# Kernel tuning notes

Hardware: AMD Instinct MI355X
Metric: run time of the kernel (lower is better)

Reference implementation:

```python
import jax, jax.numpy as jnp
import numpy as np

B, K, M, L = 16, 256, 16, 64
DET_C, HID, H, DEPTH = 1152, 128, 4, 2
DK = HID // H
SCALE = np.float32(1.0 / np.sqrt(DK))


def _ln(x, g, b):
    mu = jnp.mean(x, -1, keepdims=True)
    v = jnp.mean((x - mu) ** 2, -1, keepdims=True)
    return (x - mu) * jax.lax.rsqrt(v + 1e-5) * g + b


def _bn(x, g, b, m, v):  # eval-mode BatchNorm1d, channel-last
    return (x - m) * (g * jax.lax.rsqrt(v + 1e-5)) + b


def _prelu(x, a):
    return jnp.where(x >= 0, x, a * x)


def _mha(q_in, k_in, v_in, Wq, bq, Wk, bk, Wv, bv, Wo, bo, lg, lb, bias=None, mask=None):
    # MultiHeadAttention: scaled dot-product + residual + LayerNorm (eval, no dropout)
    Bb, Nq, _ = q_in.shape
    Nk = k_in.shape[1]
    q = (q_in @ Wq.T + bq).reshape(Bb, Nq, H, DK).transpose(0, 2, 1, 3)
    k = (k_in @ Wk.T + bk).reshape(Bb, Nk, H, DK).transpose(0, 2, 1, 3)
    v = (v_in @ Wv.T + bv).reshape(Bb, Nk, H, DK).transpose(0, 2, 1, 3)
    att = jnp.einsum('bhqd,bhkd->bhqk', q, k) * SCALE
    if bias is not None:
        att = att + bias  # way='add': per-head distance bias
    if mask is not None:
        att = jnp.where(mask, jnp.float32(-1e9), att)
    att = jax.nn.softmax(att, axis=-1)
    out = jnp.einsum('bhqk,bhkd->bhqd', att, v).transpose(0, 2, 1, 3).reshape(Bb, Nq, HID)
    out = out @ Wo.T + bo
    return _ln(q_in + out, lg, lb)


def setup_inputs() -> dict:
    key = jax.random.key(0)
    ks = iter(jax.random.split(key, 64))
    def nrm(shape, s=0.05):
        return jax.random.normal(next(ks), shape, jnp.float32) * s
    d = {}
    d['center'] = jax.random.normal(next(ks), (B, K, 3), jnp.float32)
    d['detr_features'] = nrm((B, K, DET_C), 1.0)
    d['lang_fea'] = nrm((B * M, L, HID), 1.0)
    d['fc_W1'] = nrm((HID, DET_C)); d['fc_b1'] = jnp.zeros((HID,), jnp.float32)
    for pre in ['bn1', 'mbn1', 'mbn2']:
        d[pre + '_g'] = jnp.ones((HID,), jnp.float32)
        d[pre + '_b'] = jnp.zeros((HID,), jnp.float32)
        d[pre + '_m'] = jnp.zeros((HID,), jnp.float32)
        d[pre + '_v'] = jnp.ones((HID,), jnp.float32)
    d['pr1_a'] = 0.25 * jnp.ones((HID,), jnp.float32)
    d['fc_W2'] = nrm((HID, HID)); d['fc_b2'] = jnp.zeros((HID,), jnp.float32)
    for pre in ['sa', 'ca']:
        for nm in ['Wq', 'Wk', 'Wv', 'Wo']:
            d[f'{pre}_{nm}'] = nrm((DEPTH, HID, HID))
        for nm in ['bq', 'bk', 'bv', 'bo', 'lb']:
            d[f'{pre}_{nm}'] = jnp.zeros((DEPTH, HID), jnp.float32)
        d[f'{pre}_lg'] = jnp.ones((DEPTH, HID), jnp.float32)
    d['m_W1'] = nrm((HID, HID)); d['m_b1'] = jnp.zeros((HID,), jnp.float32)
    d['mp1_a'] = 0.25 * jnp.ones((1,), jnp.float32)
    d['m_W2'] = nrm((HID, HID)); d['m_b2'] = jnp.zeros((HID,), jnp.float32)
    d['mp2_a'] = 0.25 * jnp.ones((1,), jnp.float32)
    d['m_W3'] = nrm((1, HID)); d['m_b3'] = jnp.zeros((1,), jnp.float32)
    d['attention_mask'] = jax.random.bernoulli(next(ks), 0.2, (B * M, 1, 1, L))
    d['len_nun_max'] = M
    return d


def reference(center, detr_features, lang_fea,
              fc_W1, fc_b1, bn1_g, bn1_b, bn1_m, bn1_v, pr1_a, fc_W2, fc_b2,
              sa_Wq, sa_bq, sa_Wk, sa_bk, sa_Wv, sa_bv, sa_Wo, sa_bo, sa_lg, sa_lb,
              ca_Wq, ca_bq, ca_Wk, ca_bk, ca_Wv, ca_bv, ca_Wo, ca_bo, ca_lg, ca_lb,
              m_W1, m_b1, mbn1_g, mbn1_b, mbn1_m, mbn1_v, mp1_a,
              m_W2, m_b2, mbn2_g, mbn2_b, mbn2_m, mbn2_v, mp2_a,
              m_W3, m_b3, attention_mask, len_nun_max):
    # distance-based attention bias (detached in the original)
    c = jax.lax.stop_gradient(center)
    dist = jnp.sqrt(jnp.sum((c[:, None, :, :] - c[:, :, None, :]) ** 2, -1))[:, None]  # (B,1,K,K)
    dw = 1.0 / (dist + 0.01)
    dw = dw / jnp.sum(dw, axis=2, keepdims=True)
    zeros = jnp.zeros_like(dw)
    dist_weights = jnp.concatenate([dw, -dist, zeros, zeros], axis=1)  # (B,H,K,K), one bias per head

    # features_concat: Conv1d(1x1) + BN + PReLU + Conv1d(1x1), channel-last
    x = detr_features @ fc_W1.T + fc_b1
    x = _prelu(_bn(x, bn1_g, bn1_b, bn1_m, bn1_v), pr1_a)
    x = x @ fc_W2.T + fc_b2  # (B,K,HID)

    feats = _mha(x, x, x, sa_Wq[0], sa_bq[0], sa_Wk[0], sa_bk[0], sa_Wv[0], sa_bv[0],
                 sa_Wo[0], sa_bo[0], sa_lg[0], sa_lb[0], bias=dist_weights)

    m = int(len_nun_max)
    feats = jnp.broadcast_to(feats[:, None], (B, m, K, HID)).reshape(B * m, K, HID)
    dwb = jnp.broadcast_to(dist_weights[:, None], (B, m, H, K, K)).reshape(B * m, H, K, K)

    f1 = _mha(feats, lang_fea, lang_fea, ca_Wq[0], ca_bq[0], ca_Wk[0], ca_bk[0], ca_Wv[0],
              ca_bv[0], ca_Wo[0], ca_bo[0], ca_lg[0], ca_lb[0], mask=attention_mask)
    for i in range(1, DEPTH):
        f1 = _mha(f1, f1, f1, sa_Wq[i], sa_bq[i], sa_Wk[i], sa_bk[i], sa_Wv[i], sa_bv[i],
                  sa_Wo[i], sa_bo[i], sa_lg[i], sa_lb[i], bias=dwb)
        f1 = _mha(f1, lang_fea, lang_fea, ca_Wq[i], ca_bq[i], ca_Wk[i], ca_bk[i], ca_Wv[i],
                  ca_bv[i], ca_Wo[i], ca_bo[i], ca_lg[i], ca_lb[i], mask=attention_mask)

    # match head: conv1x1+BN+PReLU x2 + conv1x1 -> 1
    y = f1 @ m_W1.T + m_b1
    y = _prelu(_bn(y, mbn1_g, mbn1_b, mbn1_m, mbn1_v), mp1_a)
    y = y @ m_W2.T + m_b2
    y = _prelu(_bn(y, mbn2_g, mbn2_b, mbn2_m, mbn2_v), mp2_a)
    conf = (y @ m_W3.T + m_b3)[..., 0]  # (B*M, K) cluster_ref
    return conf
```

## Files before the change

kernel.cpp:

```cpp
#include <hip/hip_runtime.h>
#include <hip/hip_bf16.h>
#include <cstdio>

#define KQ   256
#define HID  128
typedef unsigned short u16;
#define SCALE_F 0.1767766952966369f

typedef __bf16 bf16x8 __attribute__((ext_vector_type(8)));
typedef short  s16x8  __attribute__((ext_vector_type(8)));
typedef float  f32x4  __attribute__((ext_vector_type(4)));

static __device__ __forceinline__ float bfu(u16 u) {
    return __uint_as_float(((unsigned)u) << 16);
}
static __device__ __forceinline__ u16 f2b(float f) {
    unsigned u = __float_as_uint(f);
    return (u16)((u + 0x7FFFu + ((u >> 16) & 1u)) >> 16);
}
static __device__ __forceinline__ float ldf(const void* p, int i, int f) {
    return f ? ((const float*)p)[i] : bfu(((const u16*)p)[i]);
}
static __device__ __forceinline__ f32x4 mfma16(s16x8 a, s16x8 b, f32x4 c) {
    return __builtin_amdgcn_mfma_f32_16x16x32_bf16(
        __builtin_bit_cast(bf16x8, a), __builtin_bit_cast(bf16x8, b), c, 0, 0, 0);
}

#define OFF_WB     8256
#define OFF_LANGB  237632
#define OFF_DWB    1286208
#define OFF_DIST   2334784
#define OFF_ROWS   3383360
#define OFF_FEATSB 3387456
#define OFF_FAB    3649600
#define OFF_QB     7843904
#define OFF_KB     12038208
#define OFF_VB     16232512
#define OFF_MASK   20426816
#define NEEDF      20430912

#define WB_FCW1 0
#define WB_FCW2 147456
#define WB_SAWQ 163840
#define WB_SAWK 196608
#define WB_SAWV 229376
#define WB_SAWO 262144
#define WB_CAWQ 294912
#define WB_CAWK 327680
#define WB_CAWV 360448
#define WB_CAWO 393216
#define WB_MW1  425984
#define WB_MW2  442368

__global__ __launch_bounds__(256) void k_detect(
    const unsigned* __restrict__ onesw, const unsigned* __restrict__ maskw,
    int* __restrict__ flags)
{
    __shared__ int fb;
    if (threadIdx.x == 0) fb = 0;
    __syncthreads();
    int any = 0;
    for (int i = threadIdx.x; i < 4096; i += 256) any |= (maskw[i] > 1u) ? 1 : 0;
    if (any) atomicOr(&fb, 1);
    __syncthreads();
    if (threadIdx.x == 0) {
        flags[0] = (onesw[0] == 0x3F800000u) ? 1 : 0;
        flags[1] = fb;
    }
}

__global__ __launch_bounds__(256) void k_mask_canon(
    const unsigned char* __restrict__ raw, const int* __restrict__ flags,
    unsigned char* __restrict__ mask8)
{
    int i = blockIdx.x*256 + threadIdx.x;
    if (flags[1]) mask8[i] = raw[i] ? 1 : 0;
    else          mask8[i] = (((const unsigned int*)raw)[i] != 0u) ? 1 : 0;
}

__global__ __launch_bounds__(256) void k_cv16(
    const void* __restrict__ src, u16* __restrict__ dst, int n,
    const int* __restrict__ flags)
{
    int i = (blockIdx.x*256 + threadIdx.x)*4;
    if (i >= n) return;
    if (flags[0]) {
        float4 v = *(const float4*)((const float*)src + i);
        ushort4 o; o.x = f2b(v.x); o.y = f2b(v.y); o.z = f2b(v.z); o.w = f2b(v.w);
        *(ushort4*)(dst + i) = o;
    } else {
        *(ushort4*)(dst + i) = *(const ushort4*)((const u16*)src + i);
    }
}

__global__ __launch_bounds__(256) void k_rowsum(
    const void* __restrict__ center, float* __restrict__ rowsum,
    const int* __restrict__ flags)
{
    int f  = flags[0];
    int bi = blockIdx.x, b = bi >> 8, j = threadIdx.x;
    float cx = ldf(center, bi*3+0, f), cy = ldf(center, bi*3+1, f), cz = ldf(center, bi*3+2, f);
    int pj = (b << 8) + j;
    float px = ldf(center, pj*3+0, f), py = ldf(center, pj*3+1, f), pz = ldf(center, pj*3+2, f);
    float dx = px-cx, dy = py-cy, dz = pz-cz;
    float d  = sqrtf(dx*dx + dy*dy + dz*dz);
    float w  = 1.f/(d + 0.01f);
    float sw = w;
    #pragma unroll
    for (int m = 32; m >= 1; m >>= 1) sw += __shfl_xor(sw, m);
    __shared__ float red[4];
    if ((j & 63) == 0) red[j >> 6] = sw;
    __syncthreads();
    if (j == 0) rowsum[bi] = red[0] + red[1] + red[2] + red[3];
}

template<int EPI, bool ABCAST, bool RBCAST>
__global__ __launch_bounds__(256) void k_gemm(
    const u16* __restrict__ A, const u16* __restrict__ W, u16* __restrict__ C,
    int Kd, const void* __restrict__ bias,
    const void* __restrict__ bng, const void* __restrict__ bnb,
    const void* __restrict__ bnm, const void* __restrict__ bnv,
    const void* __restrict__ pa,
    const void* __restrict__ lg, const void* __restrict__ lb,
    const u16* __restrict__ resid, const int* __restrict__ flags, int voff)
{
    __shared__ __align__(16) u16 Wl[128*136];
    int f = flags[0];
    int t = threadIdx.x, w = t>>6, lane = t&63, lm = lane&15, q4 = lane>>4;
    int m0 = blockIdx.x*64;
    int arow = m0 + w*16 + lm;
    int grow = ABCAST ? (((arow>>12)<<8)|(arow&255)) : arow;
    const u16* Abase = A + (size_t)grow*Kd;
    f32x4 acc[8];
    #pragma unroll
    for (int nt = 0; nt < 8; ++nt) acc[nt] = f32x4{0.f,0.f,0.f,0.f};
    int sr = t>>1, ss = (t&1)*64;
    for (int k0 = 0; k0 < Kd; k0 += 128) {
        const u16* src = W + (size_t)sr*Kd + k0 + ss;
        u16* dst = Wl + sr*136 + ss;
        #pragma unroll
        for (int i = 0; i < 8; ++i) *(s16x8*)(dst + i*8) = *(const s16x8*)(src + i*8);
        __syncthreads();
        s16x8 aF[4];
        #pragma unroll
        for (int ks = 0; ks < 4; ++ks) aF[ks] = *(const s16x8*)(Abase + k0 + ks*32 + q4*8);
        #pragma unroll
        for (int nt = 0; nt < 8; ++nt)
            #pragma unroll
            for (int ks = 0; ks < 4; ++ks) {
                s16x8 bF = *(const s16x8*)(Wl + (nt*16+lm)*136 + ks*32 + q4*8);
                acc[nt] = mfma16(aF[ks], bF, acc[nt]);
            }
        __syncthreads();
    }
    int row = m0 + w*16 + q4*4;
    if (EPI == 3) {
        float xs[8][4];
        #pragma unroll
        for (int nt = 0; nt < 8; ++nt) {
            int ch = nt*16 + lm;
            float bs = ldf(bias, voff + ch, f);
            #pragma unroll
            for (int r = 0; r < 4; ++r) {
                int rr = row + r;
                int rrow = RBCAST ? (((rr>>12)<<8)|(rr&255)) : rr;
                xs[nt][r] = acc[nt][r] + bs + bfu(resid[(size_t)rrow*HID + ch]);
            }
        }
        #pragma unroll
        for (int r = 0; r < 4; ++r) {
            float sm = 0.f, sq = 0.f;
            #pragma unroll
            for (int nt = 0; nt < 8; ++nt) { sm += xs[nt][r]; sq += xs[nt][r]*xs[nt][r]; }
            #pragma unroll
            for (int d = 1; d <= 8; d <<= 1) { sm += __shfl_xor(sm, d); sq += __shfl_xor(sq, d); }
            float mean = sm * (1.f/128.f);
            float var  = sq * (1.f/128.f) - mean*mean;
            float rs   = rsqrtf(var + 1e-5f);
            #pragma unroll
            for (int nt = 0; nt < 8; ++nt) {
                int ch = nt*16 + lm;
                float g = ldf(lg, voff + ch, f), bb = ldf(lb, voff + ch, f);
                C[(size_t)(row+r)*HID + ch] = f2b((xs[nt][r]-mean)*rs*g + bb);
            }
        }
    } else {
        #pragma unroll
        for (int nt = 0; nt < 8; ++nt) {
            int ch = nt*16 + lm;
            float bs = ldf(bias, voff + ch, f);
            float scl = 1.f, sh = 0.f, al = 0.f;
            if (EPI >= 1) {
                float g  = ldf(bng, ch, f), bb = ldf(bnb, ch, f);
                float mn = ldf(bnm, ch, f), vv = ldf(bnv, ch, f);
                scl = g * rsqrtf(vv + 1e-5f);
                sh  = bb - mn*scl;
                al  = (EPI == 2) ? ldf(pa, 0, f) : ldf(pa, ch, f);
            }
            #pragma unroll
            for (int r = 0; r < 4; ++r) {
                float x = acc[nt][r] + bs;
                if (EPI >= 1) { x = x*scl + sh; x = (x >= 0.f) ? x : al*x; }
                C[(size_t)(row+r)*HID + ch] = f2b(x);
            }
        }
    }
}

__global__ __launch_bounds__(256) void k_sattn(
    const u16* __restrict__ Q, const u16* __restrict__ K, const u16* __restrict__ V,
    u16* __restrict__ O, const void* __restrict__ center,
    const float* __restrict__ rowsum, const int* __restrict__ flags, int bdiv)
{
    __shared__ __align__(16) u16 Kl[256*40];
    __shared__ __align__(16) u16 Vt[32*264];
    __shared__ __align__(16) u16 P[4][16*264];
    __shared__ float cxl[256], cyl[256], czl[256], rsl[256];
    int s = blockIdx.x, h = blockIdx.y;
    int t = threadIdx.x, w = t>>6, lane = t&63, lm = lane&15, q4 = lane>>4;
    int f = flags[0];
    int b = s / bdiv;
    {
        const u16* src = K + ((size_t)s*KQ + t)*HID + h*32;
        u16* dst = Kl + t*40;
        #pragma unroll
        for (int i = 0; i < 4; ++i) *(s16x8*)(dst + i*8) = *(const s16x8*)(src + i*8);
    }
    for (int idx = t; idx < 256*8; idx += 256) {
        int k = idx >> 3, d4 = idx & 7;
        ushort4 u = *(const ushort4*)(V + ((size_t)s*KQ + k)*HID + h*32 + d4*4);
        Vt[(d4*4+0)*264 + k] = u.x;
        Vt[(d4*4+1)*264 + k] = u.y;
        Vt[(d4*4+2)*264 + k] = u.z;
        Vt[(d4*4+3)*264 + k] = u.w;
    }
    {
        int j = (b << 8) + t;
        cxl[t] = ldf(center, j*3+0, f);
        cyl[t] = ldf(center, j*3+1, f);
        czl[t] = ldf(center, j*3+2, f);
        rsl[t] = rowsum[j];
    }
    __syncthreads();
    u16* Pw = P[w];
    for (int qt = 0; qt < 4; ++qt) {
        int qrow0 = qt*64 + w*16;
        s16x8 aq = *(const s16x8*)(Q + ((size_t)s*KQ + qrow0 + lm)*HID + h*32 + q4*8);
        float qx[4], qy[4], qz[4];
        if (h < 2) {
            #pragma unroll
            for (int r = 0; r < 4; ++r) {
                int q = qrow0 + q4*4 + r;
                qx[r] = cxl[q]; qy[r] = cyl[q]; qz[r] = czl[q];
            }
        }
        float S[16][4];
        #pragma unroll
        for (int kt = 0; kt < 16; ++kt) {
            s16x8 bF = *(const s16x8*)(Kl + (kt*16+lm)*40 + q4*8);
            f32x4 acc = f32x4{0.f,0.f,0.f,0.f};
            acc = mfma16(aq, bF, acc);
            int key = kt*16 + lm;
            float kx = 0.f, ky = 0.f, kz = 0.f, rs_ = 1.f;
            if (h < 2) { kx = cxl[key]; ky = cyl[key]; kz = czl[key]; rs_ = rsl[key]; }
            #pragma unroll
            for (int r = 0; r < 4; ++r) {
                float sc = acc[r]*SCALE_F;
                if (h < 2) {
                    float dx = qx[r]-kx, dy = qy[r]-ky, dz = qz[r]-kz;
                    float d  = sqrtf(dx*dx + dy*dy + dz*dz);
                    if (h == 0) sc += (1.f/(d + 0.01f)) / rs_;
                    else        sc -= d;
                }
                S[kt][r] = sc;
            }
        }
        float l[4];
        #pragma unroll
        for (int r = 0; r < 4; ++r) {
            float m = -3.0e38f;
            #pragma unroll
            for (int kt = 0; kt < 16; ++kt) m = fmaxf(m, S[kt][r]);
            #pragma unroll
            for (int d = 1; d <= 8; d <<= 1) m = fmaxf(m, __shfl_xor(m, d));
            float sum = 0.f;
            #pragma unroll
            for (int kt = 0; kt < 16; ++kt) { float p = __expf(S[kt][r]-m); S[kt][r] = p; sum += p; }
            #pragma unroll
            for (int d = 1; d <= 8; d <<= 1) sum += __shfl_xor(sum, d);
            l[r] = sum;
        }
        #pragma unroll
        for (int kt = 0; kt < 16; ++kt)
            #pragma unroll
            for (int r = 0; r < 4; ++r)
                Pw[(q4*4+r)*264 + kt*16 + lm] = f2b(S[kt][r]);
        #pragma unroll
        for (int nt = 0; nt < 2; ++nt) {
            f32x4 acc = f32x4{0.f,0.f,0.f,0.f};
            #pragma unroll
            for (int ks = 0; ks < 8; ++ks) {
                s16x8 ap = *(const s16x8*)(Pw + lm*264 + ks*32 + q4*8);
                s16x8 bv = *(const s16x8*)(Vt + (nt*16+lm)*264 + ks*32 + q4*8);
                acc = mfma16(ap, bv, acc);
            }
            #pragma unroll
            for (int r = 0; r < 4; ++r)
                O[((size_t)s*KQ + qrow0 + q4*4 + r)*HID + h*32 + nt*16 + lm] = f2b(acc[r] / l[r]);
        }
    }
}

__global__ __launch_bounds__(256) void k_xattn(
    const u16* __restrict__ Q, const u16* __restrict__ K, const u16* __restrict__ V,
    u16* __restrict__ O, const unsigned char* __restrict__ mask)
{
    __shared__ __align__(16) u16 Kl[64*40];
    __shared__ __align__(16) u16 Vt[32*72];
    __shared__ __align__(16) u16 P[4][16*72];
    __shared__ float madd[64];
    int s = blockIdx.x, h = blockIdx.y;
    int t = threadIdx.x, w = t>>6, lane = t&63, lm = lane&15, q4 = lane>>4;
    if (t < 64) {
        const u16* src = K + ((size_t)s*64 + t)*HID + h*32;
        u16* dst = Kl + t*40;
        #pragma unroll
        for (int i = 0; i < 4; ++i) *(s16x8*)(dst + i*8) = *(const s16x8*)(src + i*8);
        madd[t] = mask[s*64 + t] ? -1.0e9f : 0.f;
    }
    for (int idx = t; idx < 64*8; idx += 256) {
        int k = idx >> 3, d4 = idx & 7;
        ushort4 u = *(const ushort4*)(V + ((size_t)s*64 + k)*HID + h*32 + d4*4);
        Vt[(d4*4+0)*72 + k] = u.x;
        Vt[(d4*4+1)*72 + k] = u.y;
        Vt[(d4*4+2)*72 + k] = u.z;
        Vt[(d4*4+3)*72 + k] = u.w;
    }
    __syncthreads();
    u16* Pw = P[w];
    for (int qt = 0; qt < 4; ++qt) {
        int qrow0 = qt*64 + w*16;
        s16x8 aq = *(const s16x8*)(Q + ((size_t)s*KQ + qrow0 + lm)*HID + h*32 + q4*8);
        float S[4][4];
        #pragma unroll
        for (int kt = 0; kt < 4; ++kt) {
            s16x8 bF = *(const s16x8*)(Kl + (kt*16+lm)*40 + q4*8);
            f32x4 acc = f32x4{0.f,0.f,0.f,0.f};
            acc = mfma16(aq, bF, acc);
            float ma = madd[kt*16 + lm];
            #pragma unroll
            for (int r = 0; r < 4; ++r) S[kt][r] = acc[r]*SCALE_F + ma;
        }
        float l[4];
        #pragma unroll
        for (int r = 0; r < 4; ++r) {
            float m = -3.0e38f;
            #pragma unroll
            for (int kt = 0; kt < 4; ++kt) m = fmaxf(m, S[kt][r]);
            #pragma unroll
            for (int d = 1; d <= 8; d <<= 1) m = fmaxf(m, __shfl_xor(m, d));
            float sum = 0.f;
            #pragma unroll
            for (int kt = 0; kt < 4; ++kt) { float p = __expf(S[kt][r]-m); S[kt][r] = p; sum += p; }
            #pragma unroll
            for (int d = 1; d <= 8; d <<= 1) sum += __shfl_xor(sum, d);
            l[r] = sum;
        }
        #pragma unroll
        for (int kt = 0; kt < 4; ++kt)
            #pragma unroll
            for (int r = 0; r < 4; ++r)
                Pw[(q4*4+r)*72 + kt*16 + lm] = f2b(S[kt][r]);
        #pragma unroll
        for (int nt = 0; nt < 2; ++nt) {
            f32x4 acc = f32x4{0.f,0.f,0.f,0.f};
            #pragma unroll
            for (int ks = 0; ks < 2; ++ks) {
                s16x8 ap = *(const s16x8*)(Pw + lm*72 + ks*32 + q4*8);
                s16x8 bv = *(const s16x8*)(Vt + (nt*16+lm)*72 + ks*32 + q4*8);
                acc = mfma16(ap, bv, acc);
            }
            #pragma unroll
            for (int r = 0; r < 4; ++r)
                O[((size_t)s*KQ + qrow0 + q4*4 + r)*HID + h*32 + nt*16 + lm] = f2b(acc[r] / l[r]);
        }
    }
}

__global__ __launch_bounds__(256) void k_final(
    const u16* __restrict__ Y, const void* __restrict__ w3,
    const void* __restrict__ b3, void* __restrict__ outp,
    const int* __restrict__ flags)
{
    int f = flags[0];
    int w = threadIdx.x >> 6, lane = threadIdx.x & 63;
    int row = blockIdx.x*4 + w;
    float p = bfu(Y[(size_t)row*HID + lane])*ldf(w3, lane, f)
            + bfu(Y[(size_t)row*HID + 64 + lane])*ldf(w3, 64+lane, f);
    #pragma unroll
    for (int m = 32; m >= 1; m >>= 1) p += __shfl_xor(p, m);
    if (lane == 0) {
        float r = p + ldf(b3, 0, f);
        if (f) ((float*)outp)[row] = r;
        else   ((u16*)outp)[row]   = f2b(r);
    }
}

extern "C" void kernel_launch(void* const* d_in, const int* in_sizes, int n_in,
                              void* d_out, int out_size, void* d_ws, size_t ws_size,
                              hipStream_t stream)
{
    (void)n_in;
    if (ws_size < (size_t)NEEDF * 4) {
        fprintf(stderr, "kernel_launch: ws too small: have %zu need %zu\n",
                ws_size, (size_t)NEEDF * 4);
        hipMemsetAsync(d_out, 0, (size_t)out_size * 2, stream);
        return;
    }
    float* F = (float*)d_ws;
    u16*   U = (u16*)d_ws;
    int* flags = (int*)d_ws;
    u16* WB     = U + (size_t)OFF_WB*2;
    u16* langb  = U + (size_t)OFF_LANGB*2;
    u16* detrb  = U + (size_t)OFF_KB*2;
    u16* featsb = U + (size_t)OFF_FEATSB*2;
    u16* x2b    = U + (size_t)OFF_FAB*2;
    u16* fAb    = U + (size_t)OFF_FAB*2;
    u16* x1b    = U + (size_t)OFF_VB*2;
    u16* Qb     = U + (size_t)OFF_QB*2;
    u16* Kb     = U + (size_t)OFF_KB*2;
    u16* Vb     = U + (size_t)OFF_VB*2;
    float* rowsum = F + OFF_ROWS;
    unsigned char* mask8 = (unsigned char*)(F + OFF_MASK);

    k_detect<<<1, 256, 0, stream>>>((const unsigned*)d_in[8],
                                    (const unsigned*)d_in[48], flags);
    k_mask_canon<<<64, 256, 0, stream>>>((const unsigned char*)d_in[48], flags, mask8);

    struct { int idx; u16* dst; int n; } cv[14] = {
        {3,  WB+WB_FCW1, 147456}, {18, WB+WB_FCW2, 16384},
        {20, WB+WB_SAWQ, 32768}, {21, WB+WB_SAWK, 32768},
        {22, WB+WB_SAWV, 32768}, {23, WB+WB_SAWO, 32768},
        {30, WB+WB_CAWQ, 32768}, {31, WB+WB_CAWK, 32768},
        {32, WB+WB_CAWV, 32768}, {33, WB+WB_CAWO, 32768},
        {40, WB+WB_MW1, 16384},  {43, WB+WB_MW2, 16384},
        {1,  detrb, 4718592},    {2,  langb, 2097152},
    };
    for (int e = 0; e < 14; ++e)
        k_cv16<<<(cv[e].n + 1023)/1024, 256, 0, stream>>>(
            d_in[cv[e].idx], cv[e].dst, cv[e].n, flags);

    k_rowsum<<<4096, 256, 0, stream>>>(d_in[0], rowsum, flags);

    const void* N0 = nullptr;

    k_gemm<1,false,false><<<64, 256, 0, stream>>>(detrb, WB+WB_FCW1, x1b, 1152,
        d_in[4], d_in[5], d_in[6], d_in[7], d_in[8], d_in[17], N0, N0, nullptr, flags, 0);
    k_gemm<0,false,false><<<64, 256, 0, stream>>>(x1b, WB+WB_FCW2, x2b, 128,
        d_in[19], N0,N0,N0,N0,N0, N0, N0, nullptr, flags, 0);

    k_gemm<0,false,false><<<64, 256, 0, stream>>>(x2b, WB+WB_SAWQ, Qb, 128,
        d_in[24], N0,N0,N0,N0,N0, N0, N0, nullptr, flags, 0);
    k_gemm<0,false,false><<<64, 256, 0, stream>>>(x2b, WB+WB_SAWK, Kb, 128,
        d_in[25], N0,N0,N0,N0,N0, N0, N0, nullptr, flags, 0);
    k_gemm<0,false,false><<<64, 256, 0, stream>>>(x2b, WB+WB_SAWV, Vb, 128,
        d_in[26], N0,N0,N0,N0,N0, N0, N0, nullptr, flags, 0);
    k_sattn<<<dim3(16,4), 256, 0, stream>>>(Qb, Kb, Vb, Qb, d_in[0], rowsum, flags, 1);
    k_gemm<3,false,false><<<64, 256, 0, stream>>>(Qb, WB+WB_SAWO, featsb, 128,
        d_in[27], N0,N0,N0,N0,N0, d_in[29], d_in[28], x2b, flags, 0);

    k_gemm<0,true, false><<<1024, 256, 0, stream>>>(featsb, WB+WB_CAWQ, Qb, 128,
        d_in[34], N0,N0,N0,N0,N0, N0, N0, nullptr, flags, 0);
    k_gemm<0,false,false><<<256,  256, 0, stream>>>(langb, WB+WB_CAWK, Kb, 128,
        d_in[35], N0,N0,N0,N0,N0, N0, N0, nullptr, flags, 0);
    k_gemm<0,false,false><<<256,  256, 0, stream>>>(langb, WB+WB_CAWV, Vb, 128,
        d_in[36], N0,N0,N0,N0,N0, N0, N0, nullptr, flags, 0);
    k_xattn<<<dim3(256,4), 256, 0, stream>>>(Qb, Kb, Vb, Qb, mask8);
    k_gemm<3,false,true><<<1024, 256, 0, stream>>>(Qb, WB+WB_CAWO, fAb, 128,
        d_in[37], N0,N0,N0,N0,N0, d_in[39], d_in[38], featsb, flags, 0);

    k_gemm<0,false,false><<<1024, 256, 0, stream>>>(fAb, WB+WB_SAWQ+16384, Qb, 128,
        d_in[24], N0,N0,N0,N0,N0, N0, N0, nullptr, flags, 128);
    k_gemm<0,false,false><<<1024, 256, 0, stream>>>(fAb, WB+WB_SAWK+16384, Kb, 128,
        d_in[25], N0,N0,N0,N0,N0, N0, N0, nullptr, flags, 128);
    k_gemm<0,false,false><<<1024, 256, 0, stream>>>(fAb, WB+WB_SAWV+16384, Vb, 128,
        d_in[26], N0,N0,N0,N0,N0, N0, N0, nullptr, flags, 128);
    k_sattn<<<dim3(256,4), 256, 0, stream>>>(Qb, Kb, Vb, Qb, d_in[0], rowsum, flags, 16);
    k_gemm<3,false,false><<<1024, 256, 0, stream>>>(Qb, WB+WB_SAWO+16384, fAb, 128,
        d_in[27], N0,N0,N0,N0,N0, d_in[29], d_in[28], fAb, flags, 128);

    k_gemm<0,false,false><<<1024, 256, 0, stream>>>(fAb, WB+WB_CAWQ+16384, Qb, 128,
        d_in[34], N0,N0,N0,N0,N0, N0, N0, nullptr, flags, 128);
    k_gemm<0,false,false><<<256,  256, 0, stream>>>(langb, WB+WB_CAWK+16384, Kb, 128,
        d_in[35], N0,N0,N0,N0,N0, N0, N0, nullptr, flags, 128);
    k_gemm<0,false,false><<<256,  256, 0, stream>>>(langb, WB+WB_CAWV+16384, Vb, 128,
        d_in[36], N0,N0,N0,N0,N0, N0, N0, nullptr, flags, 128);
    k_xattn<<<dim3(256,4), 256, 0, stream>>>(Qb, Kb, Vb, Qb, mask8);
    k_gemm<3,false,false><<<1024, 256, 0, stream>>>(Qb, WB+WB_CAWO+16384, fAb, 128,
        d_in[37], N0,N0,N0,N0,N0, d_in[39], d_in[38], fAb, flags, 128);

    k_gemm<2,false,false><<<1024, 256, 0, stream>>>(fAb, WB+WB_MW1, Qb, 128,
        d_in[41], d_in[9], d_in[10], d_in[11], d_in[12], d_in[42], N0, N0, nullptr, flags, 0);
    k_gemm<2,false,false><<<1024, 256, 0, stream>>>(Qb, WB+WB_MW2, Kb, 128,
        d_in[44], d_in[13], d_in[14], d_in[15], d_in[16], d_in[45], N0, N0, nullptr, flags, 0);
    k_final<<<16384, 256, 0, stream>>>(Kb, d_in[46], d_in[47], d_out, flags);
}
```

Before: 614.7 us.

## Batch conversions, fuse QKV GEMMs, fold final projection into match GEMM

Replaces 14 separate conversion launches with one table-driven kernel, merges the Q/K/V (and cross-attention K/V) projection GEMMs into multi-output launches via a grid y-dimension, and fuses the final 128->1 projection into the second match-head GEMM epilogue, removing k_final. It also precomputes reciprocal row sums and swaps divisions for rcp multiplies in the attention kernels. The aim is to cut launch overhead and one full intermediate write/read, at the cost of fast-reciprocal precision and a branchy element lookup in the conversion kernel.

```diff
diff --git a/kernel.cpp b/kernel.cpp
--- a/kernel.cpp
+++ b/kernel.cpp
@@ -28,8 +28,6 @@
 
 #define OFF_WB     8256
 #define OFF_LANGB  237632
-#define OFF_DWB    1286208
-#define OFF_DIST   2334784
 #define OFF_ROWS   3383360
 #define OFF_FEATSB 3387456
 #define OFF_FAB    3649600
@@ -78,23 +76,30 @@
     else          mask8[i] = (((const unsigned int*)raw)[i] != 0u) ? 1 : 0;
 }
 
-__global__ __launch_bounds__(256) void k_cv16(
-    const void* __restrict__ src, u16* __restrict__ dst, int n,
-    const int* __restrict__ flags)
-{
-    int i = (blockIdx.x*256 + threadIdx.x)*4;
-    if (i >= n) return;
+struct CvTab {
+    const void* src[14];
+    unsigned long long dst[14];
+    int bstart[15];
+};
+__global__ __launch_bounds__(256) void k_convAll(
+    CvTab t, u16* __restrict__ U, const int* __restrict__ flags)
+{
+    int b = blockIdx.x;
+    int e = 0;
+    while (e < 13 && b >= t.bstart[e+1]) ++e;
+    long long local = (long long)(b - t.bstart[e])*1024 + threadIdx.x*4;
+    u16* dst = U + t.dst[e] + local;
     if (flags[0]) {
-        float4 v = *(const float4*)((const float*)src + i);
+        float4 v = *((const float4*)t.src[e] + (local >> 2));
         ushort4 o; o.x = f2b(v.x); o.y = f2b(v.y); o.z = f2b(v.z); o.w = f2b(v.w);
-        *(ushort4*)(dst + i) = o;
+        *(ushort4*)dst = o;
     } else {
-        *(ushort4*)(dst + i) = *(const ushort4*)((const u16*)src + i);
+        *(ushort4*)dst = *((const ushort4*)t.src[e] + (local >> 2));
     }
 }
 
 __global__ __launch_bounds__(256) void k_rowsum(
-    const void* __restrict__ center, float* __restrict__ rowsum,
+    const void* __restrict__ center, float* __restrict__ rsinv,
     const int* __restrict__ flags)
 {
     int f  = flags[0];
@@ -111,7 +116,7 @@
     __shared__ float red[4];
     if ((j & 63) == 0) red[j >> 6] = sw;
     __syncthreads();
-    if (j == 0) rowsum[bi] = red[0] + red[1] + red[2] + red[3];
+    if (j == 0) rsinv[bi] = 1.f / (red[0] + red[1] + red[2] + red[3]);
 }
 
 template<int EPI, bool ABCAST, bool RBCAST>
@@ -184,6 +189,39 @@
                 C[(size_t)(row+r)*HID + ch] = f2b((xs[nt][r]-mean)*rs*g + bb);
             }
         }
+    } else if (EPI == 4) {
+        float sum[4] = {0.f, 0.f, 0.f, 0.f};
+        float al = ldf(pa, 0, f);
+        #pragma unroll
+        for (int nt = 0; nt < 8; ++nt) {
+            int ch = nt*16 + lm;
+            float bs = ldf(bias, ch, f);
+            float g  = ldf(bng, ch, f), bb = ldf(bnb, ch, f);
+            float mn = ldf(bnm, ch, f), vv = ldf(bnv, ch, f);
+            float scl = g * rsqrtf(vv + 1e-5f);
+            float sh  = bb - mn*scl;
+            float w3v = ldf(lg, ch, f);
+            #pragma unroll
+            for (int r = 0; r < 4; ++r) {
+                float x = acc[nt][r] + bs;
+                x = x*scl + sh;
+                x = (x >= 0.f) ? x : al*x;
+                sum[r] += x * w3v;
+            }
+        }
+        #pragma unroll
+        for (int r = 0; r < 4; ++r)
+            #pragma unroll
+            for (int d = 1; d <= 8; d <<= 1) sum[r] += __shfl_xor(sum[r], d);
+        if (lm == 0) {
+            float b3v = ldf(lb, 0, f);
+            #pragma unroll
+            for (int r = 0; r < 4; ++r) {
+                float rr = sum[r] + b3v;
+                if (f) ((float*)C)[row + r] = rr;
+                else   C[row + r] = f2b(rr);
+            }
+        }
     } else {
         #pragma unroll
         for (int nt = 0; nt < 8; ++nt) {
@@ -207,10 +245,61 @@
     }
 }
 
+template<bool ABCAST>
+__global__ __launch_bounds__(256) void k_gemmN(
+    const u16* __restrict__ A,
+    const u16* __restrict__ W0, const u16* __restrict__ W1, const u16* __restrict__ W2,
+    u16* __restrict__ C0, u16* __restrict__ C1, u16* __restrict__ C2,
+    const void* __restrict__ b0, const void* __restrict__ b1, const void* __restrict__ b2,
+    const int* __restrict__ flags, int voff)
+{
+    __shared__ __align__(16) u16 Wl[128*136];
+    int y = blockIdx.y;
+    const u16* W = (y == 0) ? W0 : (y == 1) ? W1 : W2;
+    u16* C = (y == 0) ? C0 : (y == 1) ? C1 : C2;
+    const void* bias = (y == 0) ? b0 : (y == 1) ? b1 : b2;
+    int f = flags[0];
+    int t = threadIdx.x, w = t>>6, lane = t&63, lm = lane&15, q4 = lane>>4;
+    int m0 = blockIdx.x*64;
+    int arow = m0 + w*16 + lm;
+    int grow = ABCAST ? (((arow>>12)<<8)|(arow&255)) : arow;
+    const u16* Abase = A + (size_t)grow*128;
+    f32x4 acc[8];
+    #pragma unroll
+    for (int nt = 0; nt < 8; ++nt) acc[nt] = f32x4{0.f,0.f,0.f,0.f};
+    int sr = t>>1, ss = (t&1)*64;
+    {
+        const u16* src = W + (size_t)sr*128 + ss;
+        u16* dst = Wl + sr*136 + ss;
+        #pragma unroll
+        for (int i = 0; i < 8; ++i) *(s16x8*)(dst + i*8) = *(const s16x8*)(src + i*8);
+    }
+    __syncthreads();
+    s16x8 aF[4];
+    #pragma unroll
+    for (int ks = 0; ks < 4; ++ks) aF[ks] = *(const s16x8*)(Abase + ks*32 + q4*8);
+    #pragma unroll
+    for (int nt = 0; nt < 8; ++nt)
+        #pragma unroll
+        for (int ks = 0; ks < 4; ++ks) {
+            s16x8 bF = *(const s16x8*)(Wl + (nt*16+lm)*136 + ks*32 + q4*8);
+            acc[nt] = mfma16(aF[ks], bF, acc[nt]);
+        }
+    int row = m0 + w*16 + q4*4;
+    #pragma unroll
+    for (int nt = 0; nt < 8; ++nt) {
+        int ch = nt*16 + lm;
+        float bs = ldf(bias, voff + ch, f);
+        #pragma unroll
+        for (int r = 0; r < 4; ++r)
+            C[(size_t)(row+r)*HID + ch] = f2b(acc[nt][r] + bs);
+    }
+}
+
 __global__ __launch_bounds__(256) void k_sattn(
     const u16* __restrict__ Q, const u16* __restrict__ K, const u16* __restrict__ V,
     u16* __restrict__ O, const void* __restrict__ center,
-    const float* __restrict__ rowsum, const int* __restrict__ flags, int bdiv)
+    const float* __restrict__ rsinv, const int* __restrict__ flags, int bdiv)
 {
     __shared__ __align__(16) u16 Kl[256*40];
     __shared__ __align__(16) u16 Vt[32*264];
@@ -239,7 +328,7 @@
         cxl[t] = ldf(center, j*3+0, f);
         cyl[t] = ldf(center, j*3+1, f);
         czl[t] = ldf(center, j*3+2, f);
-        rsl[t] = rowsum[j];
+        rsl[t] = rsinv[j];
     }
     __syncthreads();
     u16* Pw = P[w];
@@ -269,13 +358,13 @@
                 if (h < 2) {
                     float dx = qx[r]-kx, dy = qy[r]-ky, dz = qz[r]-kz;
                     float d  = sqrtf(dx*dx + dy*dy + dz*dz);
-                    if (h == 0) sc += (1.f/(d + 0.01f)) / rs_;
+                    if (h == 0) sc += __builtin_amdgcn_rcpf(d + 0.01f) * rs_;
                     else        sc -= d;
                 }
                 S[kt][r] = sc;
             }
         }
-        float l[4];
+        float linv[4];
         #pragma unroll
         for (int r = 0; r < 4; ++r) {
             float m = -3.0e38f;
@@ -288,7 +377,7 @@
             for (int kt = 0; kt < 16; ++kt) { float p = __expf(S[kt][r]-m); S[kt][r] = p; sum += p; }
             #pragma unroll
             for (int d = 1; d <= 8; d <<= 1) sum += __shfl_xor(sum, d);
-            l[r] = sum;
+            linv[r] = __builtin_amdgcn_rcpf(sum);
         }
         #pragma unroll
         for (int kt = 0; kt < 16; ++kt)
@@ -306,7 +395,7 @@
             }
             #pragma unroll
             for (int r = 0; r < 4; ++r)
-                O[((size_t)s*KQ + qrow0 + q4*4 + r)*HID + h*32 + nt*16 + lm] = f2b(acc[r] / l[r]);
+                O[((size_t)s*KQ + qrow0 + q4*4 + r)*HID + h*32 + nt*16 + lm] = f2b(acc[r] * linv[r]);
         }
     }
 }
@@ -351,7 +440,7 @@
             #pragma unroll
             for (int r = 0; r < 4; ++r) S[kt][r] = acc[r]*SCALE_F + ma;
         }
-        float l[4];
+        float linv[4];
         #pragma unroll
         for (int r = 0; r < 4; ++r) {
             float m = -3.0e38f;
@@ -364,7 +453,7 @@
             for (int kt = 0; kt < 4; ++kt) { float p = __expf(S[kt][r]-m); S[kt][r] = p; sum += p; }
             #pragma unroll
             for (int d = 1; d <= 8; d <<= 1) sum += __shfl_xor(sum, d);
-            l[r] = sum;
+            linv[r] = __builtin_amdgcn_rcpf(sum);
         }
         #pragma unroll
         for (int kt = 0; kt < 4; ++kt)
@@ -382,27 +471,8 @@
             }
             #pragma unroll
             for (int r = 0; r < 4; ++r)
-                O[((size_t)s*KQ + qrow0 + q4*4 + r)*HID + h*32 + nt*16 + lm] = f2b(acc[r] / l[r]);
-        }
-    }
-}
-
-__global__ __launch_bounds__(256) void k_final(
-    const u16* __restrict__ Y, const void* __restrict__ w3,
-    const void* __restrict__ b3, void* __restrict__ outp,
-    const int* __restrict__ flags)
-{
-    int f = flags[0];
-    int w = threadIdx.x >> 6, lane = threadIdx.x & 63;
-    int row = blockIdx.x*4 + w;
-    float p = bfu(Y[(size_t)row*HID + lane])*ldf(w3, lane, f)
-            + bfu(Y[(size_t)row*HID + 64 + lane])*ldf(w3, 64+lane, f);
-    #pragma unroll
-    for (int m = 32; m >= 1; m >>= 1) p += __shfl_xor(p, m);
-    if (lane == 0) {
-        float r = p + ldf(b3, 0, f);
-        if (f) ((float*)outp)[row] = r;
-        else   ((u16*)outp)[row]   = f2b(r);
+                O[((size_t)s*KQ + qrow0 + q4*4 + r)*HID + h*32 + nt*16 + lm] = f2b(acc[r] * linv[r]);
+        }
     }
 }
 
@@ -430,27 +500,31 @@
     u16* Qb     = U + (size_t)OFF_QB*2;
     u16* Kb     = U + (size_t)OFF_KB*2;
     u16* Vb     = U + (size_t)OFF_VB*2;
-    float* rowsum = F + OFF_ROWS;
+    float* rsinv = F + OFF_ROWS;
     unsigned char* mask8 = (unsigned char*)(F + OFF_MASK);
 
     k_detect<<<1, 256, 0, stream>>>((const unsigned*)d_in[8],
                                     (const unsigned*)d_in[48], flags);
     k_mask_canon<<<64, 256, 0, stream>>>((const unsigned char*)d_in[48], flags, mask8);
 
-    struct { int idx; u16* dst; int n; } cv[14] = {
-        {3,  WB+WB_FCW1, 147456}, {18, WB+WB_FCW2, 16384},
-        {20, WB+WB_SAWQ, 32768}, {21, WB+WB_SAWK, 32768},
-        {22, WB+WB_SAWV, 32768}, {23, WB+WB_SAWO, 32768},
-        {30, WB+WB_CAWQ, 32768}, {31, WB+WB_CAWK, 32768},
-        {32, WB+WB_CAWV, 32768}, {33, WB+WB_CAWO, 32768},
-        {40, WB+WB_MW1, 16384},  {43, WB+WB_MW2, 16384},
-        {1,  detrb, 4718592},    {2,  langb, 2097152},
-    };
-    for (int e = 0; e < 14; ++e)
-        k_cv16<<<(cv[e].n + 1023)/1024, 256, 0, stream>>>(
-            d_in[cv[e].idx], cv[e].dst, cv[e].n, flags);
-
-    k_rowsum<<<4096, 256, 0, stream>>>(d_in[0], rowsum, flags);
+    CvTab ct;
+    {
+        const int idx[14] = {3,18,20,21,22,23,30,31,32,33,40,43,1,2};
+        const unsigned long long dst[14] = {
+            (unsigned long long)OFF_WB*2 + WB_FCW1, (unsigned long long)OFF_WB*2 + WB_FCW2,
+            (unsigned long long)OFF_WB*2 + WB_SAWQ, (unsigned long long)OFF_WB*2 + WB_SAWK,
+            (unsigned long long)OFF_WB*2 + WB_SAWV, (unsigned long long)OFF_WB*2 + WB_SAWO,
+            (unsigned long long)OFF_WB*2 + WB_CAWQ, (unsigned long long)OFF_WB*2 + WB_CAWK,
+            (unsigned long long)OFF_WB*2 + WB_CAWV, (unsigned long long)OFF_WB*2 + WB_CAWO,
+            (unsigned long long)OFF_WB*2 + WB_MW1,  (unsigned long long)OFF_WB*2 + WB_MW2,
+            (unsigned long long)OFF_KB*2,           (unsigned long long)OFF_LANGB*2 };
+        const int bs[15] = {0,144,160,192,224,256,288,320,352,384,416,432,448,5056,7104};
+        for (int e = 0; e < 14; ++e) { ct.src[e] = d_in[idx[e]]; ct.dst[e] = dst[e]; }
+        for (int e = 0; e < 15; ++e) ct.bstart[e] = bs[e];
+    }
+    k_convAll<<<7104, 256, 0, stream>>>(ct, U, flags);
+
+    k_rowsum<<<4096, 256, 0, stream>>>(d_in[0], rsinv, flags);
 
     const void* N0 = nullptr;
 
@@ -459,49 +533,41 @@
     k_gemm<0,false,false><<<64, 256, 0, stream>>>(x1b, WB+WB_FCW2, x2b, 128,
         d_in[19], N0,N0,N0,N0,N0, N0, N0, nullptr, flags, 0);
 
-    k_gemm<0,false,false><<<64, 256, 0, stream>>>(x2b, WB+WB_SAWQ, Qb, 128,
-        d_in[24], N0,N0,N0,N0,N0, N0, N0, nullptr, flags, 0);
-    k_gemm<0,false,false><<<64, 256, 0, stream>>>(x2b, WB+WB_SAWK, Kb, 128,
-        d_in[25], N0,N0,N0,N0,N0, N0, N0, nullptr, flags, 0);
-    k_gemm<0,false,false><<<64, 256, 0, stream>>>(x2b, WB+WB_SAWV, Vb, 128,
-        d_in[26], N0,N0,N0,N0,N0, N0, N0, nullptr, flags, 0);
-    k_sattn<<<dim3(16,4), 256, 0, stream>>>(Qb, Kb, Vb, Qb, d_in[0], rowsum, flags, 1);
+    k_gemmN<false><<<dim3(64,3), 256, 0, stream>>>(x2b,
+        WB+WB_SAWQ, WB+WB_SAWK, WB+WB_SAWV, Qb, Kb, Vb,
+        d_in[24], d_in[25], d_in[26], flags, 0);
+    k_sattn<<<dim3(16,4), 256, 0, stream>>>(Qb, Kb, Vb, Qb, d_in[0], rsinv, flags, 1);
     k_gemm<3,false,false><<<64, 256, 0, stream>>>(Qb, WB+WB_SAWO, featsb, 128,
         d_in[27], N0,N0,N0,N0,N0, d_in[29], d_in[28], x2b, flags, 0);
 
     k_gemm<0,true, false><<<1024, 256, 0, stream>>>(featsb, WB+WB_CAWQ, Qb, 128,
         d_in[34], N0,N0,N0,N0,N0, N0, N0, nullptr, flags, 0);
-    k_gemm<0,false,false><<<256,  256, 0, stream>>>(langb, WB+WB_CAWK, Kb, 128,
-        d_in[35], N0,N0,N0,N0,N0, N0, N0, nullptr, flags, 0);
-    k_gemm<0,false,false><<<256,  256, 0, stream>>>(langb, WB+WB_CAWV, Vb, 128,
-        d_in[36], N0,N0,N0,N0,N0, N0, N0, nullptr, flags, 0);
+    k_gemmN<false><<<dim3(256,2), 256, 0, stream>>>(langb,
+        WB+WB_CAWK, WB+WB_CAWV, nullptr, Kb, Vb, nullptr,
+        d_in[35], d_in[36], nullptr, flags, 0);
     k_xattn<<<dim3(256,4), 256, 0, stream>>>(Qb, Kb, Vb, Qb, mask8);
     k_gemm<3,false,true><<<1024, 256, 0, stream>>>(Qb, WB+WB_CAWO, fAb, 128,
         d_in[37], N0,N0,N0,N0,N0, d_in[39], d_in[38], featsb, flags, 0);
 
-    k_gemm<0,false,false><<<1024, 256, 0, stream>>>(fAb, WB+WB_SAWQ+16384, Qb, 128,
-        d_in[24], N0,N0,N0,N0,N0, N0, N0, nullptr, flags, 128);
-    k_gemm<0,false,false><<<1024, 256, 0, stream>>>(fAb, WB+WB_SAWK+16384, Kb, 128,
-        d_in[25], N0,N0,N0,N0,N0, N0, N0, nullptr, flags, 128);
-    k_gemm<0,false,false><<<1024, 256, 0, stream>>>(fAb, WB+WB_SAWV+16384, Vb, 128,
-        d_in[26], N0,N0,N0,N0,N0, N0, N0, nullptr, flags, 128);
-    k_sattn<<<dim3(256,4), 256, 0, stream>>>(Qb, Kb, Vb, Qb, d_in[0], rowsum, flags, 16);
+    k_gemmN<false><<<dim3(1024,3), 256, 0, stream>>>(fAb,
+        WB+WB_SAWQ+16384, WB+WB_SAWK+16384, WB+WB_SAWV+16384, Qb, Kb, Vb,
+        d_in[24], d_in[25], d_in[26], flags, 128);
+    k_sattn<<<dim3(256,4), 256, 0, stream>>>(Qb, Kb, Vb, Qb, d_in[0], rsinv, flags, 16);
     k_gemm<3,false,false><<<1024, 256, 0, stream>>>(Qb, WB+WB_SAWO+16384, fAb, 128,
         d_in[27], N0,N0,N0,N0,N0, d_in[29], d_in[28], fAb, flags, 128);
 
     k_gemm<0,false,false><<<1024, 256, 0, stream>>>(fAb, WB+WB_CAWQ+16384, Qb, 128,
         d_in[34], N0,N0,N0,N0,N0, N0, N0, nullptr, flags, 128);
-    k_gemm<0,false,false><<<256,  256, 0, stream>>>(langb, WB+WB_CAWK+16384, Kb, 128,
-        d_in[35], N0,N0,N0,N0,N0, N0, N0, nullptr, flags, 128);
-    k_gemm<0,false,false><<<256,  256, 0, stream>>>(langb, WB+WB_CAWV+16384, Vb, 128,
-        d_in[36], N0,N0,N0,N0,N0, N0, N0, nullptr, flags, 128);
+    k_gemmN<false><<<dim3(256,2), 256, 0, stream>>>(langb,
+        WB+WB_CAWK+16384, WB+WB_CAWV+16384, nullptr, Kb, Vb, nullptr,
+        d_in[35], d_in[36], nullptr, flags, 128);
     k_xattn<<<dim3(256,4), 256, 0, stream>>>(Qb, Kb, Vb, Qb, mask8);
     k_gemm<3,false,false><<<1024, 256, 0, stream>>>(Qb, WB+WB_CAWO+16384, fAb, 128,
         d_in[37], N0,N0,N0,N0,N0, d_in[39], d_in[38], fAb, flags, 128);
 
     k_gemm<2,false,false><<<1024, 256, 0, stream>>>(fAb, WB+WB_MW1, Qb, 128,
         d_in[41], d_in[9], d_in[10], d_in[11], d_in[12], d_in[42], N0, N0, nullptr, flags, 0);
-    k_gemm<2,false,false><<<1024, 256, 0, stream>>>(Qb, WB+WB_MW2, Kb, 128,
-        d_in[44], d_in[13], d_in[14], d_in[15], d_in[16], d_in[45], N0, N0, nullptr, flags, 0);
-    k_final<<<16384, 256, 0, stream>>>(Kb, d_in[46], d_in[47], d_out, flags);
-}
+    k_gemm<4,false,false><<<1024, 256, 0, stream>>>(Qb, WB+WB_MW2, (u16*)d_out, 128,
+        d_in[44], d_in[13], d_in[14], d_in[15], d_in[16], d_in[45],
+        d_in[46], d_in[47], nullptr, flags, 0);
+}
```

Result: faster. 563.9 us (-8.3%).
